# Kernel optimization log

Measured on AMD Instinct MI355X. Metric: run time of the kernel, lower is better.

The kernel has to match this reference:

```python
import jax, jax.numpy as jnp
import numpy as np

B, S, D, H = 2, 2048, 1024, 16
HD = D // H
EPS = 1e-8


def setup_inputs() -> dict:
    key = jax.random.key(0)
    ks = jax.random.split(key, 6)
    x = jax.random.normal(ks[0], (B, S, D), jnp.float32)
    V = jax.random.normal(ks[1], (B, S, H, HD), jnp.float32)
    # binary sparsity mask [B, S, S]
    M = (jax.random.uniform(ks[2], (B, S, S)) > 0.5).astype(jnp.float32)
    # packed QKV in-projection of nn.MultiheadAttention
    in_proj_w = jax.random.normal(ks[3], (3 * D, D), jnp.float32) / np.sqrt(D).astype(np.float32)
    in_proj_b = jnp.zeros((3 * D,), jnp.float32)
    # module-level out_proj (the mha's internal out_proj is discarded)
    out_w = jax.random.normal(ks[4], (D, D), jnp.float32) / np.sqrt(D).astype(np.float32)
    out_b = jnp.zeros((D,), jnp.float32)
    return dict(x=x, V=V, M=M, in_proj_w=in_proj_w, in_proj_b=in_proj_b,
                out_w=out_w, out_b=out_b)


def reference(x, V, M, in_proj_w, in_proj_b, out_w, out_b):
    b, s, d = x.shape
    # packed QKV projection (torch MHA semantics); v-proj computed but its
    # output path (mha output) is discarded by the module, so skip it.
    qkv = x @ in_proj_w.T + in_proj_b              # [B,S,3D]
    q, k, _ = jnp.split(qkv, 3, axis=-1)
    q = q.reshape(b, s, H, HD).transpose(0, 2, 1, 3)   # [B,H,S,HD]
    k = k.reshape(b, s, H, HD).transpose(0, 2, 1, 3)
    scale = np.float32(1.0 / np.sqrt(HD))
    scores = jnp.einsum('bhsd,bhtd->bhst', q, k) * scale  # [B,H,S,S]
    A = jax.nn.softmax(scores, axis=-1)
    # mask + L1 renormalization over keys
    A_sparse = A * M[:, None, :, :]
    norm = jnp.sum(jnp.abs(A_sparse), axis=-1, keepdims=True) + EPS
    A_bar = A_sparse / norm
    # separate value tensor V: [B,S,H,HD] -> [B,H,S,HD]
    Vp = V.transpose(0, 2, 1, 3)
    out = jnp.einsum('bhst,bhtd->bhsd', A_bar, Vp)  # [B,H,S,HD]
    out = out.transpose(0, 2, 1, 3).reshape(b, s, d)
    return out @ out_w.T + out_b
```

## Files before the change

### kernel.cpp

```cpp
#include <hip/hip_runtime.h>
#include <hip/hip_bf16.h>

#define B_  2
#define S_  2048
#define D_  1024
#define H_  16
#define HD_ 64

using bf16x8  = __attribute__((ext_vector_type(8))) __bf16;
using floatx4 = __attribute__((ext_vector_type(4))) float;
using intx4   = __attribute__((ext_vector_type(4))) int;

__device__ __forceinline__ float bf2f(unsigned short u) {
  union { unsigned int i; float f; } v; v.i = ((unsigned int)u) << 16; return v.f;
}
__device__ __forceinline__ unsigned short f2bf(float f) {
  union { float f; unsigned int i; } v; v.f = f;
  unsigned int r = v.i + 0x7fffu + ((v.i >> 16) & 1u);
  return (unsigned short)(r >> 16);
}
__device__ __forceinline__ unsigned int f2bf_pk(float a, float b) {
  union { __hip_bfloat162 h2; unsigned int u; } c;
  c.h2 = __float22bfloat162_rn(make_float2(a, b));
  return c.u;
}
__device__ __forceinline__ floatx4 mfma16(bf16x8 a, bf16x8 b, floatx4 c) {
  return __builtin_amdgcn_mfma_f32_16x16x32_bf16(a, b, c, 0, 0, 0);
}
__device__ __forceinline__ void gld16(const unsigned short* g, unsigned short* l) {
  __builtin_amdgcn_global_load_lds(
      (const __attribute__((address_space(1))) unsigned int*)g,
      (__attribute__((address_space(3))) unsigned int*)l, 16, 0, 0);
}
#define SW8(row, g) ((((g) ^ ((row) & 7)) * 8))
#define SW4(row, g) ((((g) ^ (((row) >> 1) & 3)) * 8))

__global__ __launch_bounds__(256) void prep_kernel(
    const float* __restrict__ x, const float* __restrict__ w_in,
    const float* __restrict__ w_out, const float* __restrict__ V,
    const float* __restrict__ Mm,
    unsigned short* __restrict__ xb, unsigned short* __restrict__ wb,
    unsigned short* __restrict__ wob, unsigned short* __restrict__ vt,
    unsigned long long* __restrict__ mpk)
{
  __shared__ unsigned short tile[64 * 72];
  const int bid = blockIdx.x, tid = threadIdx.x;

  if (bid < 3584) {
    const float* src; unsigned short* dst; int base;
    if (bid < 2048)      { src = x;     dst = xb;  base = bid; }
    else if (bid < 3072) { src = w_in;  dst = wb;  base = bid - 2048; }
    else                 { src = w_out; dst = wob; base = bid - 3072; }
    const int i = (base * 256 + tid) * 8;
    float4 a = *(const float4*)(src + i);
    float4 b = *(const float4*)(src + i + 4);
    union { unsigned int w[4]; intx4 v; } o;
    o.w[0] = f2bf_pk(a.x, a.y); o.w[1] = f2bf_pk(a.z, a.w);
    o.w[2] = f2bf_pk(b.x, b.y); o.w[3] = f2bf_pk(b.z, b.w);
    *(intx4*)(dst + i) = o.v;
  } else if (bid < 5632) {
    const int wave = tid >> 6, lane = tid & 63;
    const int w0 = (bid - 3584) * 64 + wave * 16;
#pragma unroll 4
    for (int j = 0; j < 16; ++j) {
      float v = Mm[(size_t)(w0 + j) * 64 + lane];
      unsigned long long bl = __ballot(v != 0.0f);
      if (lane == 0) mpk[w0 + j] = bl;
    }
  } else {
    const int idx = bid - 5632;
    const int t0 = (idx & 31) * 64, h = (idx >> 5) & 15, b = idx >> 9;
    const int sr = tid >> 3, sc = (tid & 7) * 8;
    const float* src = V + ((size_t)((b * S_ + t0) * H_ + h)) * HD_;
#pragma unroll
    for (int half = 0; half < 2; ++half) {
      const int r = sr + half * 32;
      float4 v0 = *(const float4*)&src[(size_t)r * (H_ * HD_) + sc];
      float4 v1 = *(const float4*)&src[(size_t)r * (H_ * HD_) + sc + 4];
      union { unsigned int w[4]; intx4 v; } p;
      p.w[0] = f2bf_pk(v0.x, v0.y); p.w[1] = f2bf_pk(v0.z, v0.w);
      p.w[2] = f2bf_pk(v1.x, v1.y); p.w[3] = f2bf_pk(v1.z, v1.w);
      *(intx4*)&tile[r * 72 + sc] = p.v;
    }
    __syncthreads();
    unsigned short* dst = vt + ((size_t)((b * H_ + h) * HD_)) * S_ + t0;
    union { unsigned short u[8]; intx4 v; } pack;
#pragma unroll
    for (int j = 0; j < 8; ++j) pack.u[j] = tile[(sc + j) * 72 + sr];
    *(intx4*)&dst[(size_t)sr * S_ + sc] = pack.v;
#pragma unroll
    for (int j = 0; j < 8; ++j) pack.u[j] = tile[(sc + j) * 72 + sr + 32];
    *(intx4*)&dst[(size_t)(sr + 32) * S_ + sc] = pack.v;
  }
}

__global__ __launch_bounds__(256) void gemm_abt(
    const unsigned short* __restrict__ A,
    const unsigned short* __restrict__ Bm,
    const float* __restrict__ bias,
    unsigned short* __restrict__ Cb, float* __restrict__ Cf,
    int M, int N, int K, int qscale)
{
  __shared__ unsigned short As[128 * 32];
  __shared__ unsigned short Bs[128 * 32];

  const int tid  = threadIdx.x;
  const int wave = tid >> 6, lane = tid & 63;
  const int quad = lane >> 4, l15 = lane & 15;
  const int wr = wave >> 1, wc = wave & 1;
  const int bm = blockIdx.y * 128, bn = blockIdx.x * 128;
  const int srow = tid >> 2, gs = tid & 3;

  floatx4 acc[4][4];
#pragma unroll
  for (int mt = 0; mt < 4; ++mt)
#pragma unroll
    for (int nt = 0; nt < 4; ++nt)
      acc[mt][nt] = (floatx4){0.f, 0.f, 0.f, 0.f};

  for (int k0 = 0; k0 < K; k0 += 32) {
    __syncthreads();
#pragma unroll
    for (int r = 0; r < 2; ++r) {
      const int row = srow + r * 64;
      gld16(&A[(size_t)(bm + row) * K + k0 + SW4(row, gs)],
            &As[wave * 512 + r * 2048]);
      gld16(&Bm[(size_t)(bn + row) * K + k0 + SW4(row, gs)],
            &Bs[wave * 512 + r * 2048]);
    }
    __syncthreads();

    bf16x8 af[4], bf[4];
#pragma unroll
    for (int mt = 0; mt < 4; ++mt) {
      const int row = wr * 64 + mt * 16 + l15;
      af[mt] = *(const bf16x8*)&As[row * 32 + SW4(row, quad)];
    }
#pragma unroll
    for (int nt = 0; nt < 4; ++nt) {
      const int row = wc * 64 + nt * 16 + l15;
      bf[nt] = *(const bf16x8*)&Bs[row * 32 + SW4(row, quad)];
    }
#pragma unroll
    for (int mt = 0; mt < 4; ++mt)
#pragma unroll
      for (int nt = 0; nt < 4; ++nt)
        acc[mt][nt] = mfma16(af[mt], bf[nt], acc[mt][nt]);
  }

#pragma unroll
  for (int nt = 0; nt < 4; ++nt) {
    const int col = bn + wc * 64 + nt * 16 + l15;
    const float bi = bias[col];
    const float sc = (qscale && col < 1024) ? 0.125f : 1.0f;
#pragma unroll
    for (int mt = 0; mt < 4; ++mt) {
      const int row0 = bm + wr * 64 + mt * 16 + quad * 4;
#pragma unroll
      for (int reg = 0; reg < 4; ++reg) {
        const float v = (acc[mt][nt][reg] + bi) * sc;
        if (Cf) Cf[(size_t)(row0 + reg) * N + col] = v;
        else    Cb[(size_t)(row0 + reg) * N + col] = f2bf(v);
      }
    }
  }
}

__global__ __launch_bounds__(256) void attn_kernel(
    const unsigned short* __restrict__ QK,
    const unsigned short* __restrict__ Vt,
    const unsigned long long* __restrict__ Mpk,
    unsigned short* __restrict__ ctx)
{
  __shared__ unsigned short PQ[128 * 72];
  __shared__ unsigned short Ks[2][64 * 64];
  __shared__ unsigned short Vs[2][64 * 64];
  __shared__ unsigned long long Ms64[2][128];

  const int tid  = threadIdx.x;
  const int wave = tid >> 6, lane = tid & 63;
  const int quad = lane >> 4, l15 = lane & 15;
  const int b = blockIdx.z, h = blockIdx.y, qb = blockIdx.x * 128;
  const int gs = tid & 7;

  const unsigned short* Qbase = QK + (size_t)(b * S_ + qb) * 2048 + h * HD_;
  const unsigned short* Kbase = QK + (size_t)(b * S_) * 2048 + D_ + h * HD_;
  const unsigned short* Vbase = Vt + (size_t)((b * H_ + h) * HD_) * S_;
  const unsigned long long* Mbase = Mpk + (size_t)(b * S_ + qb) * (S_ / 64);

#pragma unroll
  for (int r = 0; r < 4; ++r) {
    const int row = (tid >> 3) + r * 32;
    gld16(Qbase + (size_t)row * 2048 + SW8(row, gs), &PQ[wave * 512 + r * 2048]);
  }
#pragma unroll
  for (int r = 0; r < 2; ++r) {
    const int row = (tid >> 3) + r * 32;
    gld16(Kbase + (size_t)row * 2048 + SW8(row, gs), &Ks[0][wave * 512 + r * 2048]);
    gld16(Vbase + (size_t)row * S_ + SW8(row, gs),   &Vs[0][wave * 512 + r * 2048]);
  }
  if (tid < 128) Ms64[0][tid] = Mbase[(size_t)tid * (S_ / 64)];
  asm volatile("s_waitcnt vmcnt(0)" ::: "memory");
  __syncthreads();

  bf16x8 qf[2][2];
#pragma unroll
  for (int mt = 0; mt < 2; ++mt)
#pragma unroll
    for (int c = 0; c < 2; ++c) {
      const int row = wave * 32 + mt * 16 + l15;
      qf[mt][c] = *(const bf16x8*)&PQ[row * 64 + SW8(row, c * 4 + quad)];
    }
  asm volatile("s_waitcnt lgkmcnt(0)" ::: "memory");

  floatx4 accO[2][4];
  float Pp[2][4];
#pragma unroll
  for (int mt = 0; mt < 2; ++mt)
#pragma unroll
    for (int nt = 0; nt < 4; ++nt) {
      accO[mt][nt] = (floatx4){0.f, 0.f, 0.f, 0.f};
      Pp[mt][nt] = 0.f;
    }

  for (int i = 0; i < 32; ++i) {
    const int cur = i & 1, nxt = cur ^ 1;
    asm volatile("s_waitcnt vmcnt(0)" ::: "memory");
    __syncthreads();

    if (i + 1 < 32) {
      const int t1 = (i + 1) * 64;
#pragma unroll
      for (int r = 0; r < 2; ++r) {
        const int row = (tid >> 3) + r * 32;
        gld16(Kbase + (size_t)(t1 + row) * 2048 + SW8(row, gs),
              &Ks[nxt][wave * 512 + r * 2048]);
        gld16(Vbase + (size_t)row * S_ + t1 + SW8(row, gs),
              &Vs[nxt][wave * 512 + r * 2048]);
      }
      if (tid < 128)
        Ms64[nxt][tid] = Mbase[(size_t)tid * (S_ / 64) + i + 1];
    }

    floatx4 sc[2][4];
#pragma unroll
    for (int nt = 0; nt < 4; ++nt) {
      const int row = nt * 16 + l15;
      bf16x8 kf0 = *(const bf16x8*)&Ks[cur][row * 64 + SW8(row, quad)];
      bf16x8 kf1 = *(const bf16x8*)&Ks[cur][row * 64 + SW8(row, 4 + quad)];
#pragma unroll
      for (int mt = 0; mt < 2; ++mt) {
        floatx4 z = (floatx4){0.f, 0.f, 0.f, 0.f};
        z = mfma16(qf[mt][0], kf0, z);
        z = mfma16(qf[mt][1], kf1, z);
        sc[mt][nt] = z;
      }
    }

    unsigned long long mw[2][4];
#pragma unroll
    for (int mt = 0; mt < 2; ++mt)
#pragma unroll
      for (int reg = 0; reg < 4; ++reg)
        mw[mt][reg] = Ms64[cur][wave * 32 + mt * 16 + quad * 4 + reg];

#pragma unroll
    for (int mt = 0; mt < 2; ++mt)
#pragma unroll
      for (int nt = 0; nt < 4; ++nt)
#pragma unroll
        for (int rp = 0; rp < 2; ++rp) {
          const int r0 = rp * 2, r1 = rp * 2 + 1;
          float e0 = __expf(sc[mt][nt][r0]);
          float e1 = __expf(sc[mt][nt][r1]);
          unsigned int w0 = (nt < 2) ? (unsigned int)mw[mt][r0]
                                     : (unsigned int)(mw[mt][r0] >> 32);
          unsigned int w1 = (nt < 2) ? (unsigned int)mw[mt][r1]
                                     : (unsigned int)(mw[mt][r1] >> 32);
          const int sh = (nt & 1) * 16 + l15;
          float p0 = ((w0 >> sh) & 1u) ? e0 : 0.0f;
          float p1 = ((w1 >> sh) & 1u) ? e1 : 0.0f;
          Pp[mt][r0] += p0;
          Pp[mt][r1] += p1;
          unsigned int u = f2bf_pk(p0, p1);
          const int rowA = wave * 32 + mt * 16 + quad * 4 + r0;
          const int cg = nt * 2 + (l15 >> 3), co = l15 & 7;
          PQ[rowA * 72 + SW8(rowA, cg) + co] = (unsigned short)u;
          PQ[(rowA + 1) * 72 + SW8(rowA + 1, cg) + co] = (unsigned short)(u >> 16);
        }

    asm volatile("s_waitcnt lgkmcnt(0)" ::: "memory");

    bf16x8 pf0[2], pf1[2];
#pragma unroll
    for (int mt = 0; mt < 2; ++mt) {
      const int row = wave * 32 + mt * 16 + l15;
      pf0[mt] = *(const bf16x8*)&PQ[row * 72 + SW8(row, quad)];
      pf1[mt] = *(const bf16x8*)&PQ[row * 72 + SW8(row, 4 + quad)];
    }
#pragma unroll
    for (int nt = 0; nt < 4; ++nt) {
      const int row = nt * 16 + l15;
      bf16x8 vf0 = *(const bf16x8*)&Vs[cur][row * 64 + SW8(row, quad)];
      bf16x8 vf1 = *(const bf16x8*)&Vs[cur][row * 64 + SW8(row, 4 + quad)];
#pragma unroll
      for (int mt = 0; mt < 2; ++mt) {
        accO[mt][nt] = mfma16(pf0[mt], vf0, accO[mt][nt]);
        accO[mt][nt] = mfma16(pf1[mt], vf1, accO[mt][nt]);
      }
    }
  }

#pragma unroll
  for (int off = 1; off <= 8; off <<= 1)
#pragma unroll
    for (int mt = 0; mt < 2; ++mt)
#pragma unroll
      for (int reg = 0; reg < 4; ++reg)
        Pp[mt][reg] += __shfl_xor(Pp[mt][reg], off);

#pragma unroll
  for (int mt = 0; mt < 2; ++mt)
#pragma unroll
    for (int reg = 0; reg < 4; ++reg)
      Pp[mt][reg] = 1.0f / (Pp[mt][reg] + 1e-30f);

#pragma unroll
  for (int mt = 0; mt < 2; ++mt)
#pragma unroll
    for (int nt = 0; nt < 4; ++nt)
#pragma unroll
      for (int reg = 0; reg < 4; ++reg) {
        const int row = wave * 32 + mt * 16 + quad * 4 + reg;
        ctx[(size_t)(b * S_ + qb + row) * D_ + h * HD_ + nt * 16 + l15] =
            f2bf(accO[mt][nt][reg] * Pp[mt][reg]);
      }
}

extern "C" void kernel_launch(void* const* d_in, const int* in_sizes, int n_in,
                              void* d_out, int out_size, void* d_ws, size_t ws_size,
                              hipStream_t stream) {
  const float* x     = (const float*)d_in[0];
  const float* V     = (const float*)d_in[1];
  const float* Mm    = (const float*)d_in[2];
  const float* w_in  = (const float*)d_in[3];
  const float* b_in  = (const float*)d_in[4];
  const float* w_out = (const float*)d_in[5];
  const float* b_out = (const float*)d_in[6];
  float* out = (float*)d_out;

  unsigned short* qk  = (unsigned short*)d_ws;
  unsigned short* vt  = qk  + (size_t)8 * 1024 * 1024;
  unsigned short* ctx = vt  + (size_t)4 * 1024 * 1024;
  unsigned short* xb  = ctx + (size_t)4 * 1024 * 1024;
  unsigned short* wb  = xb  + (size_t)4 * 1024 * 1024;
  unsigned short* wob = wb  + (size_t)2 * 1024 * 1024;
  unsigned long long* mpk = (unsigned long long*)(wob + (size_t)1024 * 1024);

  prep_kernel<<<6656, 256, 0, stream>>>(x, w_in, w_out, V, Mm,
                                        xb, wb, wob, vt, mpk);

  gemm_abt<<<dim3(2048 / 128, (B_ * S_) / 128), 256, 0, stream>>>(
      xb, wb, b_in, qk, nullptr, B_ * S_, 2048, D_, 1);

  attn_kernel<<<dim3(S_ / 128, H_, B_), 256, 0, stream>>>(qk, vt, mpk, ctx);

  gemm_abt<<<dim3(D_ / 128, (B_ * S_) / 128), 256, 0, stream>>>(
      ctx, wob, b_out, nullptr, out, B_ * S_, D_, D_, 0);
}
```

Measured before the change: 257.8 us.

## Keep attention probabilities in registers via transposed score MFMA and permuted K rows

Computes scores as K·Qᵀ so each lane holds scores for one query row, and loads K rows through a token permutation (TAU). That register layout then matches the A-operand layout of the P·V MFMA, so the probabilities are packed to bf16 directly in registers and the LDS round trip through the PQ buffer is removed. The Q staging buffer now aliases the K buffer, which adds a barrier before K is loaded. It also adds s_setprio around the MFMA blocks and a simpler row-sum reduction. The risk is correctness, since the TAU permutation and the mask-bit mapping must agree exactly.

```diff
diff --git a/kernel.cpp b/kernel.cpp
--- a/kernel.cpp
+++ b/kernel.cpp
@@ -11,9 +11,6 @@
 using floatx4 = __attribute__((ext_vector_type(4))) float;
 using intx4   = __attribute__((ext_vector_type(4))) int;
 
-__device__ __forceinline__ float bf2f(unsigned short u) {
-  union { unsigned int i; float f; } v; v.i = ((unsigned int)u) << 16; return v.f;
-}
 __device__ __forceinline__ unsigned short f2bf(float f) {
   union { float f; unsigned int i; } v; v.f = f;
   unsigned int r = v.i + 0x7fffu + ((v.i >> 16) & 1u);
@@ -34,6 +31,7 @@
 }
 #define SW8(row, g) ((((g) ^ ((row) & 7)) * 8))
 #define SW4(row, g) ((((g) ^ (((row) >> 1) & 3)) * 8))
+#define TAU(r) (((r) & 0x23) | (((r) & 0x08) << 1) | (((r) & 0x04) << 1) | (((r) & 0x10) >> 2))
 
 __global__ __launch_bounds__(256) void prep_kernel(
     const float* __restrict__ x, const float* __restrict__ w_in,
@@ -172,7 +170,6 @@
     const unsigned long long* __restrict__ Mpk,
     unsigned short* __restrict__ ctx)
 {
-  __shared__ unsigned short PQ[128 * 72];
   __shared__ unsigned short Ks[2][64 * 64];
   __shared__ unsigned short Vs[2][64 * 64];
   __shared__ unsigned long long Ms64[2][128];
@@ -188,16 +185,11 @@
   const unsigned short* Vbase = Vt + (size_t)((b * H_ + h) * HD_) * S_;
   const unsigned long long* Mbase = Mpk + (size_t)(b * S_ + qb) * (S_ / 64);
 
+  unsigned short* Qs = &Ks[0][0];
 #pragma unroll
   for (int r = 0; r < 4; ++r) {
     const int row = (tid >> 3) + r * 32;
-    gld16(Qbase + (size_t)row * 2048 + SW8(row, gs), &PQ[wave * 512 + r * 2048]);
-  }
-#pragma unroll
-  for (int r = 0; r < 2; ++r) {
-    const int row = (tid >> 3) + r * 32;
-    gld16(Kbase + (size_t)row * 2048 + SW8(row, gs), &Ks[0][wave * 512 + r * 2048]);
-    gld16(Vbase + (size_t)row * S_ + SW8(row, gs),   &Vs[0][wave * 512 + r * 2048]);
+    gld16(Qbase + (size_t)row * 2048 + SW8(row, gs), Qs + wave * 512 + r * 2048);
   }
   if (tid < 128) Ms64[0][tid] = Mbase[(size_t)tid * (S_ / 64)];
   asm volatile("s_waitcnt vmcnt(0)" ::: "memory");
@@ -209,19 +201,29 @@
 #pragma unroll
     for (int c = 0; c < 2; ++c) {
       const int row = wave * 32 + mt * 16 + l15;
-      qf[mt][c] = *(const bf16x8*)&PQ[row * 64 + SW8(row, c * 4 + quad)];
-    }
-  asm volatile("s_waitcnt lgkmcnt(0)" ::: "memory");
+      qf[mt][c] = *(const bf16x8*)&Qs[row * 64 + SW8(row, c * 4 + quad)];
+    }
+  __syncthreads();
+
+#pragma unroll
+  for (int r = 0; r < 2; ++r) {
+    const int rowd = (tid >> 3) + r * 32;
+    const int tokK = TAU(rowd);
+    gld16(Kbase + (size_t)tokK * 2048 + SW8(rowd, gs), &Ks[0][wave * 512 + r * 2048]);
+    gld16(Vbase + (size_t)rowd * S_ + SW8(rowd, gs),   &Vs[0][wave * 512 + r * 2048]);
+  }
+
+  unsigned int bmask[8];
+#pragma unroll
+  for (int j = 0; j < 8; ++j) bmask[j] = 1u << (quad * 8 + j);
 
   floatx4 accO[2][4];
-  float Pp[2][4];
+  float Pp[2] = {0.f, 0.f};
 #pragma unroll
   for (int mt = 0; mt < 2; ++mt)
 #pragma unroll
-    for (int nt = 0; nt < 4; ++nt) {
+    for (int nt = 0; nt < 4; ++nt)
       accO[mt][nt] = (floatx4){0.f, 0.f, 0.f, 0.f};
-      Pp[mt][nt] = 0.f;
-    }
 
   for (int i = 0; i < 32; ++i) {
     const int cur = i & 1, nxt = cur ^ 1;
@@ -232,17 +234,19 @@
       const int t1 = (i + 1) * 64;
 #pragma unroll
       for (int r = 0; r < 2; ++r) {
-        const int row = (tid >> 3) + r * 32;
-        gld16(Kbase + (size_t)(t1 + row) * 2048 + SW8(row, gs),
+        const int rowd = (tid >> 3) + r * 32;
+        const int tokK = TAU(rowd);
+        gld16(Kbase + (size_t)(t1 + tokK) * 2048 + SW8(rowd, gs),
               &Ks[nxt][wave * 512 + r * 2048]);
-        gld16(Vbase + (size_t)row * S_ + t1 + SW8(row, gs),
+        gld16(Vbase + (size_t)rowd * S_ + t1 + SW8(rowd, gs),
               &Vs[nxt][wave * 512 + r * 2048]);
       }
       if (tid < 128)
         Ms64[nxt][tid] = Mbase[(size_t)tid * (S_ / 64) + i + 1];
     }
 
-    floatx4 sc[2][4];
+    floatx4 sc[4][2];
+    __builtin_amdgcn_s_setprio(1);
 #pragma unroll
     for (int nt = 0; nt < 4; ++nt) {
       const int row = nt * 16 + l15;
@@ -251,79 +255,75 @@
 #pragma unroll
       for (int mt = 0; mt < 2; ++mt) {
         floatx4 z = (floatx4){0.f, 0.f, 0.f, 0.f};
-        z = mfma16(qf[mt][0], kf0, z);
-        z = mfma16(qf[mt][1], kf1, z);
-        sc[mt][nt] = z;
-      }
-    }
-
-    unsigned long long mw[2][4];
+        z = mfma16(kf0, qf[mt][0], z);
+        z = mfma16(kf1, qf[mt][1], z);
+        sc[nt][mt] = z;
+      }
+    }
+    __builtin_amdgcn_s_setprio(0);
+
+    unsigned long long mw[2];
 #pragma unroll
     for (int mt = 0; mt < 2; ++mt)
-#pragma unroll
-      for (int reg = 0; reg < 4; ++reg)
-        mw[mt][reg] = Ms64[cur][wave * 32 + mt * 16 + quad * 4 + reg];
-
-#pragma unroll
-    for (int mt = 0; mt < 2; ++mt)
-#pragma unroll
-      for (int nt = 0; nt < 4; ++nt)
-#pragma unroll
-        for (int rp = 0; rp < 2; ++rp) {
-          const int r0 = rp * 2, r1 = rp * 2 + 1;
-          float e0 = __expf(sc[mt][nt][r0]);
-          float e1 = __expf(sc[mt][nt][r1]);
-          unsigned int w0 = (nt < 2) ? (unsigned int)mw[mt][r0]
-                                     : (unsigned int)(mw[mt][r0] >> 32);
-          unsigned int w1 = (nt < 2) ? (unsigned int)mw[mt][r1]
-                                     : (unsigned int)(mw[mt][r1] >> 32);
-          const int sh = (nt & 1) * 16 + l15;
-          float p0 = ((w0 >> sh) & 1u) ? e0 : 0.0f;
-          float p1 = ((w1 >> sh) & 1u) ? e1 : 0.0f;
-          Pp[mt][r0] += p0;
-          Pp[mt][r1] += p1;
-          unsigned int u = f2bf_pk(p0, p1);
-          const int rowA = wave * 32 + mt * 16 + quad * 4 + r0;
-          const int cg = nt * 2 + (l15 >> 3), co = l15 & 7;
-          PQ[rowA * 72 + SW8(rowA, cg) + co] = (unsigned short)u;
-          PQ[(rowA + 1) * 72 + SW8(rowA + 1, cg) + co] = (unsigned short)(u >> 16);
-        }
-
-    asm volatile("s_waitcnt lgkmcnt(0)" ::: "memory");
-
-    bf16x8 pf0[2], pf1[2];
-#pragma unroll
-    for (int mt = 0; mt < 2; ++mt) {
-      const int row = wave * 32 + mt * 16 + l15;
-      pf0[mt] = *(const bf16x8*)&PQ[row * 72 + SW8(row, quad)];
-      pf1[mt] = *(const bf16x8*)&PQ[row * 72 + SW8(row, 4 + quad)];
-    }
+      mw[mt] = Ms64[cur][wave * 32 + mt * 16 + l15];
+
+    bf16x8 vf0[4], vf1[4];
 #pragma unroll
     for (int nt = 0; nt < 4; ++nt) {
       const int row = nt * 16 + l15;
-      bf16x8 vf0 = *(const bf16x8*)&Vs[cur][row * 64 + SW8(row, quad)];
-      bf16x8 vf1 = *(const bf16x8*)&Vs[cur][row * 64 + SW8(row, 4 + quad)];
+      vf0[nt] = *(const bf16x8*)&Vs[cur][row * 64 + SW8(row, quad)];
+      vf1[nt] = *(const bf16x8*)&Vs[cur][row * 64 + SW8(row, 4 + quad)];
+    }
+
+    bf16x8 pa0[2], pa1[2];
+#pragma unroll
+    for (int mt = 0; mt < 2; ++mt) {
+      const unsigned int mlo = (unsigned int)mw[mt];
+      const unsigned int mhi = (unsigned int)(mw[mt] >> 32);
+      union { unsigned int w[4]; bf16x8 v; } A0, A1;
+#pragma unroll
+      for (int nt = 0; nt < 4; ++nt) {
+        const unsigned int word = (nt < 2) ? mlo : mhi;
+        float p[4];
+#pragma unroll
+        for (int reg = 0; reg < 4; ++reg) {
+          const float e = __expf(sc[nt][mt][reg]);
+          p[reg] = (word & bmask[(nt & 1) * 4 + reg]) ? e : 0.0f;
+        }
+        Pp[mt] += (p[0] + p[1]) + (p[2] + p[3]);
+        const unsigned int d0 = f2bf_pk(p[0], p[1]);
+        const unsigned int d1 = f2bf_pk(p[2], p[3]);
+        if (nt == 0)      { A0.w[0] = d0; A0.w[1] = d1; }
+        else if (nt == 1) { A0.w[2] = d0; A0.w[3] = d1; }
+        else if (nt == 2) { A1.w[0] = d0; A1.w[1] = d1; }
+        else              { A1.w[2] = d0; A1.w[3] = d1; }
+      }
+      pa0[mt] = A0.v; pa1[mt] = A1.v;
+    }
+
+    __builtin_amdgcn_s_setprio(1);
+#pragma unroll
+    for (int nt = 0; nt < 4; ++nt)
 #pragma unroll
       for (int mt = 0; mt < 2; ++mt) {
-        accO[mt][nt] = mfma16(pf0[mt], vf0, accO[mt][nt]);
-        accO[mt][nt] = mfma16(pf1[mt], vf1, accO[mt][nt]);
-      }
-    }
-  }
-
-#pragma unroll
-  for (int off = 1; off <= 8; off <<= 1)
-#pragma unroll
-    for (int mt = 0; mt < 2; ++mt)
-#pragma unroll
-      for (int reg = 0; reg < 4; ++reg)
-        Pp[mt][reg] += __shfl_xor(Pp[mt][reg], off);
-
+        accO[mt][nt] = mfma16(pa0[mt], vf0[nt], accO[mt][nt]);
+        accO[mt][nt] = mfma16(pa1[mt], vf1[nt], accO[mt][nt]);
+      }
+    __builtin_amdgcn_s_setprio(0);
+  }
+
+#pragma unroll
+  for (int mt = 0; mt < 2; ++mt) {
+    Pp[mt] += __shfl_xor(Pp[mt], 16);
+    Pp[mt] += __shfl_xor(Pp[mt], 32);
+    Pp[mt] = 1.0f / (Pp[mt] + 1e-30f);
+  }
+  float Ppe[2][4];
 #pragma unroll
   for (int mt = 0; mt < 2; ++mt)
 #pragma unroll
     for (int reg = 0; reg < 4; ++reg)
-      Pp[mt][reg] = 1.0f / (Pp[mt][reg] + 1e-30f);
+      Ppe[mt][reg] = __shfl(Pp[mt], (quad << 4) | (quad * 4 + reg));
 
 #pragma unroll
   for (int mt = 0; mt < 2; ++mt)
@@ -333,7 +333,7 @@
       for (int reg = 0; reg < 4; ++reg) {
         const int row = wave * 32 + mt * 16 + quad * 4 + reg;
         ctx[(size_t)(b * S_ + qb + row) * D_ + h * HD_ + nt * 16 + l15] =
-            f2bf(accO[mt][nt][reg] * Pp[mt][reg]);
+            f2bf(accO[mt][nt][reg] * Ppe[mt][reg]);
       }
 }
 
```

After: 250.7 us. 2.8% less time.
